# Kernel tuning notes

Hardware: AMD Instinct MI355X
Metric: run time of the kernel (lower is better)

The kernel has to match this reference:

```python
import jax, jax.numpy as jnp
import numpy as np

B, S, H, NH, HD = 2, 2048, 2048, 16, 128


def _bit_linear(x, w):
    """Ternary STE BitLinear: absmean scaling, round/clamp, fp matmul, rescale."""
    eps = 1e-5
    wn = w / (jnp.abs(w).mean() + eps)
    # straight-through estimator: forward uses quantized weights, grad flows to wn
    wq = wn + jax.lax.stop_gradient(jnp.clip(jnp.round(wn), -1.0, 1.0) - wn)
    y = x @ wq.T
    scale = w.shape[1]  # in_features
    Qb = 128.0  # 2**(8-1)
    return jnp.clip(y / scale * Qb, -Qb, Qb)


def _rotate_half(x):
    x1, x2 = jnp.split(x, 2, axis=-1)
    return jnp.concatenate([-x2, x1], axis=-1)


def setup_inputs() -> dict:
    key = jax.random.key(0)
    k1, k2, k3 = jax.random.split(key, 3)
    x = jax.random.normal(k1, (B, S, H), dtype=jnp.float32)
    w_qkv = jax.random.normal(k2, (3 * H, H), dtype=jnp.float32) * 0.02
    w_o = jax.random.normal(k3, (H, H), dtype=jnp.float32) * 0.02
    # realistic RoPE table [2, S, HD]
    inv_freq = 1.0 / (10000.0 ** (jnp.arange(0, HD, 2, dtype=jnp.float32) / HD))
    freqs = jnp.arange(S, dtype=jnp.float32)[:, None] * inv_freq[None, :]
    emb = jnp.concatenate([freqs, freqs], axis=-1)  # [S, HD]
    rotary = jnp.stack([jnp.cos(emb), jnp.sin(emb)], axis=0)
    return {"x": x, "rotary": rotary, "w_qkv": w_qkv, "w_o": w_o}


def reference(x, rotary, w_qkv, w_o):
    qkv = _bit_linear(x, w_qkv)  # [B, S, 3H]
    q, k, v = jnp.split(qkv, 3, axis=-1)
    q = q.reshape(B, S, NH, HD)
    k = k.reshape(B, S, NH, HD)
    v = v.reshape(B, S, NH, HD)
    cos = rotary[0][None, :, None, :]  # [1, S, 1, HD]
    sin = rotary[1][None, :, None, :]
    q = q * cos + _rotate_half(q) * sin
    k = k * cos + _rotate_half(k) * sin
    # [B, NH, S, HD]
    q, k, v = (t.transpose(0, 2, 1, 3) for t in (q, k, v))
    scores = jnp.einsum("bhqd,bhkd->bhqk", q, k) / np.sqrt(HD).astype(np.float32)
    causal = jnp.tril(jnp.ones((S, S), dtype=bool))
    scores = jnp.where(causal[None, None], scores, -jnp.inf)
    attn = jax.nn.softmax(scores, axis=-1)
    y = jnp.einsum("bhqk,bhkd->bhqd", attn, v)
    y = y.transpose(0, 2, 1, 3).reshape(B, S, H)
    return _bit_linear(y, w_o)
```

## Files before the change

### kernel.cpp

```cpp
#include <hip/hip_runtime.h>
#include <hip/hip_bf16.h>
#include <stdint.h>

#define B_   2
#define S_   2048
#define H_   2048
#define NH_  16
#define HD_  128
#define MTOK 4096
#define NQKV 6144

typedef unsigned short u16;
typedef __attribute__((ext_vector_type(8))) __bf16 bf16x8;
typedef __attribute__((ext_vector_type(4))) float f32x4;
typedef __attribute__((ext_vector_type(16))) float f32x16;

static __device__ __forceinline__ float bf2f(u16 u){
  union { uint32_t i; float f; } v; v.i = ((uint32_t)u) << 16; return v.f;
}
static __device__ __forceinline__ u16 f2bf(float f){
  union { float f; uint32_t i; } v; v.f = f;
  uint32_t r = v.i + 0x7FFFu + ((v.i >> 16) & 1u);
  return (u16)(r >> 16);
}
static __device__ __forceinline__ uint32_t cvt_pk_bf16(float lo, float hi){
  uint32_t r;
  asm("v_cvt_pk_bf16_f32 %0, %1, %2" : "=v"(r) : "v"(lo), "v"(hi));
  return r;
}
static __device__ __forceinline__ void pl32swap(uint32_t &a, uint32_t &b){
  asm volatile("v_permlane32_swap_b32 %0, %1" : "+v"(a), "+v"(b));
}

__device__ __forceinline__ void gload_lds16(const void* g, void* l){
  __builtin_amdgcn_global_load_lds((const __attribute__((address_space(1))) void*)g,
                                   (__attribute__((address_space(3))) void*)l, 16, 0, 0);
}

__global__ void absum_kernel(const float* __restrict__ w, int n, float* __restrict__ partial){
  __shared__ float sm[256];
  float s = 0.f;
  for (int i = blockIdx.x*256 + threadIdx.x; i < n; i += gridDim.x*256)
    s += fabsf(w[i]);
  sm[threadIdx.x] = s; __syncthreads();
  for (int st = 128; st > 0; st >>= 1){
    if ((int)threadIdx.x < st) sm[threadIdx.x] += sm[threadIdx.x + st];
    __syncthreads();
  }
  if (threadIdx.x == 0) partial[blockIdx.x] = sm[0];
}

__global__ void finalize_kernel(const float* __restrict__ p1, const float* __restrict__ p2,
                                float* __restrict__ scales){
  __shared__ double sm[256];
  int t = threadIdx.x;
  double s = (double)p1[t] + (double)p1[t+256] + (double)p1[t+512] + (double)p1[t+768];
  sm[t] = s; __syncthreads();
  for (int st = 128; st > 0; st >>= 1){ if (t < st) sm[t] += sm[t+st]; __syncthreads(); }
  if (t == 0) scales[0] = (float)(1.0 / (sm[0] / (double)(3*H_*H_) + 1e-5));
  __syncthreads();
  s = (double)p2[t] + (double)p2[t+256] + (double)p2[t+512] + (double)p2[t+768];
  sm[t] = s; __syncthreads();
  for (int st = 128; st > 0; st >>= 1){ if (t < st) sm[t] += sm[t+st]; __syncthreads(); }
  if (t == 0) scales[1] = (float)(1.0 / (sm[0] / (double)(H_*H_) + 1e-5));
}

__global__ void quant_kernel(const float* __restrict__ w, u16* __restrict__ wq, int n,
                             const float* __restrict__ scales, int which){
  float inv = scales[which];
  for (int i = blockIdx.x*256 + threadIdx.x; i < n; i += gridDim.x*256){
    float q = rintf(w[i] * inv);
    q = fminf(1.f, fmaxf(-1.f, q));
    wq[i] = f2bf(q);
  }
}

__global__ void castx_kernel(const float* __restrict__ x, u16* __restrict__ xb, int n){
  int i = blockIdx.x*256 + threadIdx.x;
  if (i < n) xb[i] = f2bf(x[i]);
}

template<int EPI>
__global__ __launch_bounds__(512, 2) void gemm_kernel(const u16* __restrict__ A,
    const u16* __restrict__ Bw, int M, int N, int K,
    float* __restrict__ outf, u16* __restrict__ qb, u16* __restrict__ kb, u16* __restrict__ vtb)
{
  extern __shared__ u16 lds[];
  int nbm = M >> 7;
  int nb_tot = nbm * (N >> 8);
  int bid = blockIdx.x;
  int chunk = nb_tot >> 3;
  int sb = (bid & 7)*chunk + (bid >> 3);
  int bm = sb % nbm, bn = sb / nbm;
  int m0 = bm << 7, n0 = bn << 8;
  int tid = threadIdx.x;
  int lane = tid & 63, wid = tid >> 6;
  int wm = wid >> 2, wn = wid & 3;
  int lr = lane & 15, lg = lane >> 4;
  int lg8 = lg << 3;
  int kw = (wid & 1) << 5;

  const u16* Ab = A + (size_t)m0 * K;
  const u16* Bb = Bw + (size_t)n0 * K;

  f32x4 acc[4][4];
  #pragma unroll
  for (int i = 0; i < 4; i++)
    #pragma unroll
    for (int j = 0; j < 4; j++) acc[i][j] = f32x4{0.f,0.f,0.f,0.f};

  auto STAGE = [&](int tt, int vlo){
    u16* ldst = lds + (tt % 3) * 24576;
    int k0 = tt << 6;
    #pragma unroll
    for (int v = vlo; v < vlo + 3; v++){
      int f = v*8 + wid;
      const u16* src;
      if (v < 2){
        src = Ab + (size_t)(((f >> 1) << 4) + lr)*K + k0 + kw + lg8;
      } else {
        src = Bb + (size_t)((((f - 16) >> 1) << 4) + lr)*K + k0 + kw + lg8;
      }
      gload_lds16(src, ldst + f*512 + lane*8);
    }
  };

  int NT = K >> 6;
  STAGE(0,0); STAGE(0,3); STAGE(1,0); STAGE(1,3);
  asm volatile("s_waitcnt vmcnt(6)" ::: "memory");
  __builtin_amdgcn_sched_barrier(0);
  __builtin_amdgcn_s_barrier();

  for (int t = 0; t < NT; t++){
    u16* bufp = lds + (t % 3) * 24576;
    #pragma unroll
    for (int ph = 0; ph < 2; ph++){
      if (t + 2 < NT) STAGE(t + 2, ph*3);
      bf16x8 af[4], bfr[4];
      #pragma unroll
      for (int mi = 0; mi < 4; mi++)
        af[mi] = *(const bf16x8*)(bufp + (((wm*4 + mi)*2 + ph)*512) + lane*8);
      #pragma unroll
      for (int ni = 0; ni < 4; ni++)
        bfr[ni] = *(const bf16x8*)(bufp + ((16 + (wn*4 + ni)*2 + ph)*512) + lane*8);
      __builtin_amdgcn_s_setprio(1);
      #pragma unroll
      for (int mi = 0; mi < 4; mi++)
        #pragma unroll
        for (int ni = 0; ni < 4; ni++)
          acc[mi][ni] = __builtin_amdgcn_mfma_f32_16x16x32_bf16(af[mi], bfr[ni], acc[mi][ni], 0, 0, 0);
      __builtin_amdgcn_s_setprio(0);
      if (ph == 0){
        __builtin_amdgcn_s_barrier();
      } else {
        if (t + 2 < NT) asm volatile("s_waitcnt vmcnt(6)" ::: "memory");
        else            asm volatile("s_waitcnt vmcnt(0)" ::: "memory");
        __builtin_amdgcn_sched_barrier(0);
        __builtin_amdgcn_s_barrier();
      }
    }
  }

  #pragma unroll
  for (int mi = 0; mi < 4; mi++){
    #pragma unroll
    for (int ni = 0; ni < 4; ni++){
      int ncol = n0 + wn*64 + ni*16 + lr;
      #pragma unroll
      for (int r = 0; r < 4; r++){
        int m = m0 + wm*64 + mi*16 + lg*4 + r;
        float v = acc[mi][ni][r] * 0.0625f;
        v = fminf(128.f, fmaxf(-128.f, v));
        if (EPI == 1){
          outf[(size_t)m*N + ncol] = v;
        } else {
          int b = m >> 11, s = m & 2047;
          int part = ncol >> 11, c = ncol & 2047;
          int h = c >> 7, d = c & 127;
          int bh = b*NH_ + h;
          u16 bv = f2bf(v);
          if (part == 0)      qb[((bh*S_ + s) << 7) + d] = bv;
          else if (part == 1) kb[((bh*S_ + s) << 7) + d] = bv;
          else                vtb[((bh*HD_ + d) << 11) + s] = bv;
        }
      }
    }
  }
}

__global__ void rope_kernel(u16* __restrict__ qb, u16* __restrict__ kb, const float* __restrict__ rot){
  int i = blockIdx.x*256 + threadIdx.x;
  int d = i & 63;
  int s = (i >> 6) & 2047;
  int bh = (i >> 17) & 31;
  u16* buf = (i >> 22) ? kb : qb;
  int base = (bh*S_ + s)*HD_;
  float c  = rot[s*HD_ + d];
  float sn = rot[S_*HD_ + s*HD_ + d];
  float x1 = bf2f(buf[base + d]);
  float x2 = bf2f(buf[base + d + 64]);
  buf[base + d]      = f2bf(x1*c - x2*sn);
  buf[base + d + 64] = f2bf(x2*c + x1*sn);
}

__global__ __launch_bounds__(256) void attn_kernel(const u16* __restrict__ qb,
    const u16* __restrict__ kb, const u16* __restrict__ vtb, u16* __restrict__ ao)
{
  __shared__ alignas(16) u16 Ks[2][4096];
  __shared__ alignas(16) u16 Vs[2][4096];

  int bid = blockIdx.x;
  int sbid = (bid & 7)*64 + (bid >> 3);
  int bh = sbid >> 4;
  int bq = 15 - (sbid & 15);
  int tid = threadIdx.x;
  int wid = tid >> 6, lane = tid & 63;
  int l31 = lane & 31, hl = lane >> 5;
  int q0 = bq * 128;
  int qw = q0 + wid*32;
  int q  = qw + l31;

  const u16* Qp = qb + (size_t)(bh*S_ + qw)*HD_;
  const u16* Kp = kb + (size_t)bh*S_*HD_;
  const u16* Vt = vtb + (size_t)bh*HD_*S_;

  bf16x8 qf[8];
  #pragma unroll
  for (int t = 0; t < 8; t++)
    qf[t] = *(const bf16x8*)(Qp + l31*HD_ + t*16 + hl*8);

  f32x16 o[4];
  #pragma unroll
  for (int i = 0; i < 4; i++)
    #pragma unroll
    for (int j = 0; j < 16; j++) o[i][j] = 0.f;
  float m_r = -1e30f, l_r = 0.f;
  const float sm_scale = 0.08838834764831845f;

  auto STAGE = [&](int buf, int kt2){
    int t0 = wid*2;
    gload_lds16(Kp + (size_t)(kt2 + l31)*HD_ + (t0  )*16 + hl*8, &Ks[buf][((t0  )*64 + lane)*8]);
    gload_lds16(Kp + (size_t)(kt2 + l31)*HD_ + (t0+1)*16 + hl*8, &Ks[buf][((t0+1)*64 + lane)*8]);
    int v0 = wid*2, v1 = wid*2 + 1;
    gload_lds16(Vt + (size_t)((v0&3)*32 + l31)*S_ + kt2 + (v0>>2)*16 + hl*8, &Vs[buf][(v0*64 + lane)*8]);
    gload_lds16(Vt + (size_t)((v1&3)*32 + l31)*S_ + kt2 + (v1>>2)*16 + hl*8, &Vs[buf][(v1*64 + lane)*8]);
  };

  int n_it = 4*bq + 4;
  STAGE(0, 0);
  int cur = 0, kt = 0;
  for (int it = 0; it < n_it; ++it, kt += 32){
    if (it + 1 < n_it){
      STAGE(cur ^ 1, kt + 32);
      asm volatile("s_waitcnt vmcnt(4)" ::: "memory");
    } else {
      asm volatile("s_waitcnt vmcnt(0)" ::: "memory");
    }
    __builtin_amdgcn_sched_barrier(0);
    __builtin_amdgcn_s_barrier();

    if (kt <= qw){
      f32x16 sa;
      #pragma unroll
      for (int j = 0; j < 16; j++) sa[j] = 0.f;
      #pragma unroll
      for (int t = 0; t < 8; t++){
        bf16x8 kf = *(const bf16x8*)(&Ks[cur][(t*64 + lane)*8]);
        sa = __builtin_amdgcn_mfma_f32_32x32x16_bf16(kf, qf[t], sa, 0, 0, 0);
      }

      float sv[16];
      if (kt == qw){
        #pragma unroll
        for (int r = 0; r < 16; r++){
          int key = kt + (r&3) + 8*(r>>2) + 4*hl;
          sv[r] = (key > q) ? -1e30f : sa[r]*sm_scale;
        }
      } else {
        #pragma unroll
        for (int r = 0; r < 16; r++) sv[r] = sa[r]*sm_scale;
      }

      float pm = sv[0];
      #pragma unroll
      for (int r = 1; r < 16; r++) pm = fmaxf(pm, sv[r]);
      pm = fmaxf(pm, __shfl_xor(pm, 32));
      if (!__all(pm - m_r <= 8.f)){
        float mn = fmaxf(m_r, pm);
        float scl = __expf(m_r - mn);
        m_r = mn; l_r *= scl;
        #pragma unroll
        for (int i = 0; i < 4; i++)
          #pragma unroll
          for (int j = 0; j < 16; j++) o[i][j] *= scl;
      }
      float p[16];
      #pragma unroll
      for (int r = 0; r < 16; r++) p[r] = __expf(sv[r] - m_r);
      float ts = 0.f;
      #pragma unroll
      for (int r = 0; r < 16; r++) ts += p[r];
      ts += __shfl_xor(ts, 32);
      l_r += ts;

      uint32_t a0 = cvt_pk_bf16(p[0],  p[1]),  a1 = cvt_pk_bf16(p[2],  p[3]);
      uint32_t a2 = cvt_pk_bf16(p[4],  p[5]),  a3 = cvt_pk_bf16(p[6],  p[7]);
      uint32_t b0 = cvt_pk_bf16(p[8],  p[9]),  b1 = cvt_pk_bf16(p[10], p[11]);
      uint32_t b2 = cvt_pk_bf16(p[12], p[13]), b3 = cvt_pk_bf16(p[14], p[15]);
      pl32swap(a0, a2); pl32swap(a1, a3);
      pl32swap(b0, b2); pl32swap(b1, b3);
      union { uint32_t u[4]; bf16x8 v; } pf0, pf1;
      pf0.u[0]=a0; pf0.u[1]=a1; pf0.u[2]=a2; pf0.u[3]=a3;
      pf1.u[0]=b0; pf1.u[1]=b1; pf1.u[2]=b2; pf1.u[3]=b3;

      #pragma unroll
      for (int db = 0; db < 4; db++){
        bf16x8 vf0 = *(const bf16x8*)(&Vs[cur][((0*4 + db)*64 + lane)*8]);
        o[db] = __builtin_amdgcn_mfma_f32_32x32x16_bf16(vf0, pf0.v, o[db], 0, 0, 0);
        bf16x8 vf1 = *(const bf16x8*)(&Vs[cur][((1*4 + db)*64 + lane)*8]);
        o[db] = __builtin_amdgcn_mfma_f32_32x32x16_bf16(vf1, pf1.v, o[db], 0, 0, 0);
      }
      asm volatile("s_waitcnt lgkmcnt(0)" ::: "memory");
    }
    __builtin_amdgcn_sched_barrier(0);
    __builtin_amdgcn_s_barrier();
    cur ^= 1;
  }

  float inv = 1.f / l_r;
  int b = bh >> 4, hh = bh & 15;
  u16* orow = ao + (size_t)(b*S_ + q)*H_ + hh*HD_;
  #pragma unroll
  for (int db = 0; db < 4; db++){
    #pragma unroll
    for (int g = 0; g < 4; g++){
      ushort4 pk4;
      pk4.x = f2bf(o[db][4*g+0]*inv);
      pk4.y = f2bf(o[db][4*g+1]*inv);
      pk4.z = f2bf(o[db][4*g+2]*inv);
      pk4.w = f2bf(o[db][4*g+3]*inv);
      *(ushort4*)(orow + db*32 + g*8 + hl*4) = pk4;
    }
  }
}

extern "C" void kernel_launch(void* const* d_in, const int* in_sizes, int n_in,
                              void* d_out, int out_size, void* d_ws, size_t ws_size,
                              hipStream_t stream) {
  const float* x      = (const float*)d_in[0];
  const float* rotary = (const float*)d_in[1];
  const float* w_qkv  = (const float*)d_in[2];
  const float* w_o    = (const float*)d_in[3];
  float* out = (float*)d_out;

  char* wsb = (char*)d_ws;
  float* part_qkv = (float*)wsb;
  float* part_o   = part_qkv + 1024;
  float* scales   = part_o + 1024;
  size_t off = 16384;
  u16* xb    = (u16*)(wsb + off); off += (size_t)MTOK*H_*2;
  u16* wqkvq = (u16*)(wsb + off); off += (size_t)NQKV*H_*2;
  u16* woq   = (u16*)(wsb + off); off += (size_t)H_*H_*2;
  u16* qbuf  = (u16*)(wsb + off); off += (size_t)B_*NH_*S_*HD_*2;
  u16* kbuf  = (u16*)(wsb + off); off += (size_t)B_*NH_*S_*HD_*2;
  u16* vtb   = (u16*)(wsb + off); off += (size_t)B_*NH_*S_*HD_*2;
  u16* ao    = (u16*)(wsb + off); off += (size_t)MTOK*H_*2;

  const int GEMM_LDS = 3 * 48 * 1024;
  hipFuncSetAttribute((const void*)&gemm_kernel<0>,
                      hipFuncAttributeMaxDynamicSharedMemorySize, GEMM_LDS);
  hipFuncSetAttribute((const void*)&gemm_kernel<1>,
                      hipFuncAttributeMaxDynamicSharedMemorySize, GEMM_LDS);

  absum_kernel<<<1024, 256, 0, stream>>>(w_qkv, 3*H_*H_, part_qkv);
  absum_kernel<<<1024, 256, 0, stream>>>(w_o, H_*H_, part_o);
  finalize_kernel<<<1, 256, 0, stream>>>(part_qkv, part_o, scales);
  quant_kernel<<<4096, 256, 0, stream>>>(w_qkv, wqkvq, 3*H_*H_, scales, 0);
  quant_kernel<<<2048, 256, 0, stream>>>(w_o, woq, H_*H_, scales, 1);
  castx_kernel<<<(MTOK*H_)/256, 256, 0, stream>>>(x, xb, MTOK*H_);

  gemm_kernel<0><<<(MTOK/128)*(NQKV/256), 512, GEMM_LDS, stream>>>(xb, wqkvq, MTOK, NQKV, H_,
                                                                   nullptr, qbuf, kbuf, vtb);
  rope_kernel<<<(2*B_*NH_*S_*64)/256, 256, 0, stream>>>(qbuf, kbuf, rotary);
  attn_kernel<<<B_*NH_*(S_/128), 256, 0, stream>>>(qbuf, kbuf, vtb, ao);
  gemm_kernel<1><<<(MTOK/128)*(H_/256), 512, GEMM_LDS, stream>>>(ao, woq, MTOK, H_, H_,
                                                                 out, nullptr, nullptr, nullptr);
}
```

Baseline: 421.4 us.

## Enlarge GEMM tiles to 256x256 with double-buffered 8-wave ping-pong schedule

The bf16 GEMM goes from 128x256 to 256x256 block tiles, so each wave holds an 8x4 grid of 16x16 accumulators. The triple-buffered K=64 pipeline becomes a double-buffered even/odd LDS scheme. Global-to-LDS staging is interleaved with quarter-tile MFMA groups between barriers, with fine-grained vmcnt and lgkmcnt waits. This aims to raise arithmetic intensity and cut global traffic per FLOP, in exchange for more registers, 128KB of LDS (so likely one block per CU), fewer blocks and many extra barriers.

Result: slower. 439.5 us (+4.3%).

```diff
diff --git a/kernel.cpp b/kernel.cpp
--- a/kernel.cpp
+++ b/kernel.cpp
@@ -80,95 +80,135 @@
   if (i < n) xb[i] = f2bf(x[i]);
 }
 
+#define BARR  __builtin_amdgcn_s_barrier()
+#define LGKM0 asm volatile("s_waitcnt lgkmcnt(0)" ::: "memory")
+#define VMW4  do{ asm volatile("s_waitcnt vmcnt(4)" ::: "memory"); __builtin_amdgcn_sched_barrier(0); }while(0)
+#define VMW0  do{ asm volatile("s_waitcnt vmcnt(0)" ::: "memory"); __builtin_amdgcn_sched_barrier(0); }while(0)
+
+#define LDA4(basep, MI0) do{                                           \
+  _Pragma("unroll") for (int mi = 0; mi < 4; mi++)                     \
+    _Pragma("unroll") for (int ks = 0; ks < 2; ks++)                   \
+      aR[mi][ks] = *(const bf16x8*)((basep) +                          \
+          (((wm*8 + (MI0) + mi)*2 + ks)<<9) + (lane<<3));              \
+}while(0)
+#define LDB2(basep, DST, NI0) do{                                      \
+  _Pragma("unroll") for (int ni = 0; ni < 2; ni++)                     \
+    _Pragma("unroll") for (int ks = 0; ks < 2; ks++)                   \
+      DST[ni][ks] = *(const bf16x8*)((basep) +                         \
+          (((wn*4 + (NI0) + ni)*2 + ks)<<9) + (lane<<3));              \
+}while(0)
+#define MMQ(Aa, Bb2, MI0, NI0) do{                                     \
+  __builtin_amdgcn_s_setprio(1);                                       \
+  _Pragma("unroll") for (int ks = 0; ks < 2; ks++)                     \
+    _Pragma("unroll") for (int mi = 0; mi < 4; mi++)                   \
+      _Pragma("unroll") for (int ni = 0; ni < 2; ni++)                 \
+        acc[(MI0)+mi][(NI0)+ni] = __builtin_amdgcn_mfma_f32_16x16x32_bf16( \
+            Aa[mi][ks], Bb2[ni][ks], acc[(MI0)+mi][(NI0)+ni], 0, 0, 0);\
+  __builtin_amdgcn_s_setprio(0);                                       \
+}while(0)
+
 template<int EPI>
 __global__ __launch_bounds__(512, 2) void gemm_kernel(const u16* __restrict__ A,
     const u16* __restrict__ Bw, int M, int N, int K,
     float* __restrict__ outf, u16* __restrict__ qb, u16* __restrict__ kb, u16* __restrict__ vtb)
 {
   extern __shared__ u16 lds[];
-  int nbm = M >> 7;
+  const int AE = 0, BE = 16384, AO = 32768, BO = 49152;
+  int nbm = M >> 8;
   int nb_tot = nbm * (N >> 8);
   int bid = blockIdx.x;
   int chunk = nb_tot >> 3;
   int sb = (bid & 7)*chunk + (bid >> 3);
   int bm = sb % nbm, bn = sb / nbm;
-  int m0 = bm << 7, n0 = bn << 8;
+  int m0 = bm << 8, n0 = bn << 8;
   int tid = threadIdx.x;
   int lane = tid & 63, wid = tid >> 6;
   int wm = wid >> 2, wn = wid & 3;
   int lr = lane & 15, lg = lane >> 4;
   int lg8 = lg << 3;
-  int kw = (wid & 1) << 5;
 
   const u16* Ab = A + (size_t)m0 * K;
   const u16* Bb = Bw + (size_t)n0 * K;
 
-  f32x4 acc[4][4];
+  f32x4 acc[8][4];
   #pragma unroll
-  for (int i = 0; i < 4; i++)
+  for (int i = 0; i < 8; i++)
     #pragma unroll
     for (int j = 0; j < 4; j++) acc[i][j] = f32x4{0.f,0.f,0.f,0.f};
 
-  auto STAGE = [&](int tt, int vlo){
-    u16* ldst = lds + (tt % 3) * 24576;
-    int k0 = tt << 6;
-    #pragma unroll
-    for (int v = vlo; v < vlo + 3; v++){
-      int f = v*8 + wid;
-      const u16* src;
-      if (v < 2){
-        src = Ab + (size_t)(((f >> 1) << 4) + lr)*K + k0 + kw + lg8;
-      } else {
-        src = Bb + (size_t)((((f - 16) >> 1) << 4) + lr)*K + k0 + kw + lg8;
-      }
-      gload_lds16(src, ldst + f*512 + lane*8);
+  auto STAGE_A = [&](int T, int h){
+    u16* base = lds + ((T & 1) ? AO : AE);
+    int kt = T << 6;
+    #pragma unroll
+    for (int j = 0; j < 2; j++){
+      int fa = h*16 + wid*2 + j;
+      int m16 = fa >> 1, ks = fa & 1;
+      gload_lds16(Ab + (size_t)(m16*16 + lr)*K + kt + ks*32 + lg8,
+                  base + (fa<<9) + (lane<<3));
     }
   };
-
-  int NT = K >> 6;
-  STAGE(0,0); STAGE(0,3); STAGE(1,0); STAGE(1,3);
-  asm volatile("s_waitcnt vmcnt(6)" ::: "memory");
-  __builtin_amdgcn_sched_barrier(0);
-  __builtin_amdgcn_s_barrier();
-
-  for (int t = 0; t < NT; t++){
-    u16* bufp = lds + (t % 3) * 24576;
-    #pragma unroll
-    for (int ph = 0; ph < 2; ph++){
-      if (t + 2 < NT) STAGE(t + 2, ph*3);
-      bf16x8 af[4], bfr[4];
-      #pragma unroll
-      for (int mi = 0; mi < 4; mi++)
-        af[mi] = *(const bf16x8*)(bufp + (((wm*4 + mi)*2 + ph)*512) + lane*8);
-      #pragma unroll
-      for (int ni = 0; ni < 4; ni++)
-        bfr[ni] = *(const bf16x8*)(bufp + ((16 + (wn*4 + ni)*2 + ph)*512) + lane*8);
-      __builtin_amdgcn_s_setprio(1);
-      #pragma unroll
-      for (int mi = 0; mi < 4; mi++)
-        #pragma unroll
-        for (int ni = 0; ni < 4; ni++)
-          acc[mi][ni] = __builtin_amdgcn_mfma_f32_16x16x32_bf16(af[mi], bfr[ni], acc[mi][ni], 0, 0, 0);
-      __builtin_amdgcn_s_setprio(0);
-      if (ph == 0){
-        __builtin_amdgcn_s_barrier();
-      } else {
-        if (t + 2 < NT) asm volatile("s_waitcnt vmcnt(6)" ::: "memory");
-        else            asm volatile("s_waitcnt vmcnt(0)" ::: "memory");
-        __builtin_amdgcn_sched_barrier(0);
-        __builtin_amdgcn_s_barrier();
-      }
-    }
+  auto STAGE_B = [&](int T, int h){
+    u16* base = lds + ((T & 1) ? BO : BE);
+    int kt = T << 6;
+    #pragma unroll
+    for (int j = 0; j < 2; j++){
+      int fb = h*16 + wid*2 + j;
+      int n16 = fb >> 1, ks = fb & 1;
+      gload_lds16(Bb + (size_t)(n16*16 + lr)*K + kt + ks*32 + lg8,
+                  base + (fb<<9) + (lane<<3));
+    }
+  };
+
+  const u16* aE = lds + AE; const u16* bE = lds + BE;
+  const u16* aO = lds + AO; const u16* bO = lds + BO;
+
+  STAGE_A(0,0); STAGE_A(0,1); STAGE_B(0,0); STAGE_B(0,1);
+  STAGE_B(1,0); STAGE_A(1,0);
+  VMW4;
+  BARR;
+
+  int NITER = K >> 7;
+  for (int i = 0; i < NITER; i++){
+    bool last = (i == NITER - 1);
+    int t1 = 2*i + 1, t2 = 2*i + 2, t3 = 2*i + 3;
+    bf16x8 aR[4][2], bLo[2][2], bHi[2][2];
+
+    LDA4(aE, 0); LDB2(bE, bLo, 0);
+    STAGE_B(t1, 1);
+    BARR; LGKM0; MMQ(aR, bLo, 0, 0); BARR;
+    LDB2(bE, bHi, 2);
+    STAGE_A(t1, 1);
+    BARR; LGKM0; MMQ(aR, bHi, 0, 2); BARR;
+    LDA4(aE, 4);
+    if (!last) STAGE_B(t2, 0);
+    BARR; LGKM0; MMQ(aR, bHi, 4, 2); BARR;
+    if (!last) STAGE_A(t2, 0);
+    BARR; LGKM0; MMQ(aR, bLo, 4, 0);
+    if (!last) VMW4; else VMW0;
+    BARR;
+    LDA4(aO, 0); LDB2(bO, bLo, 0);
+    if (!last) STAGE_B(t2, 1);
+    BARR; LGKM0; MMQ(aR, bLo, 0, 0); BARR;
+    LDB2(bO, bHi, 2);
+    if (!last) STAGE_A(t2, 1);
+    BARR; LGKM0; MMQ(aR, bHi, 0, 2); BARR;
+    LDA4(aO, 4);
+    if (!last) STAGE_B(t3, 0);
+    BARR; LGKM0; MMQ(aR, bHi, 4, 2); BARR;
+    if (!last) STAGE_A(t3, 0);
+    BARR; LGKM0; MMQ(aR, bLo, 4, 0);
+    if (!last){ VMW4; }
+    BARR;
   }
 
   #pragma unroll
-  for (int mi = 0; mi < 4; mi++){
+  for (int mi = 0; mi < 8; mi++){
     #pragma unroll
     for (int ni = 0; ni < 4; ni++){
       int ncol = n0 + wn*64 + ni*16 + lr;
       #pragma unroll
       for (int r = 0; r < 4; r++){
-        int m = m0 + wm*64 + mi*16 + lg*4 + r;
+        int m = m0 + wm*128 + mi*16 + lg*4 + r;
         float v = acc[mi][ni][r] * 0.0625f;
         v = fminf(128.f, fmaxf(-128.f, v));
         if (EPI == 1){
@@ -366,7 +406,7 @@
   u16* vtb   = (u16*)(wsb + off); off += (size_t)B_*NH_*S_*HD_*2;
   u16* ao    = (u16*)(wsb + off); off += (size_t)MTOK*H_*2;
 
-  const int GEMM_LDS = 3 * 48 * 1024;
+  const int GEMM_LDS = 128 * 1024;
   hipFuncSetAttribute((const void*)&gemm_kernel<0>,
                       hipFuncAttributeMaxDynamicSharedMemorySize, GEMM_LDS);
   hipFuncSetAttribute((const void*)&gemm_kernel<1>,
@@ -379,10 +419,10 @@
   quant_kernel<<<2048, 256, 0, stream>>>(w_o, woq, H_*H_, scales, 1);
   castx_kernel<<<(MTOK*H_)/256, 256, 0, stream>>>(x, xb, MTOK*H_);
 
-  gemm_kernel<0><<<(MTOK/128)*(NQKV/256), 512, GEMM_LDS, stream>>>(xb, wqkvq, MTOK, NQKV, H_,
+  gemm_kernel<0><<<(MTOK/256)*(NQKV/256), 512, GEMM_LDS, stream>>>(xb, wqkvq, MTOK, NQKV, H_,
                                                                    nullptr, qbuf, kbuf, vtb);
   rope_kernel<<<(2*B_*NH_*S_*64)/256, 256, 0, stream>>>(qbuf, kbuf, rotary);
   attn_kernel<<<B_*NH_*(S_/128), 256, 0, stream>>>(qbuf, kbuf, vtb, ao);
-  gemm_kernel<1><<<(MTOK/128)*(H_/256), 512, GEMM_LDS, stream>>>(ao, woq, MTOK, H_, H_,
+  gemm_kernel<1><<<(MTOK/256)*(H_/256), 512, GEMM_LDS, stream>>>(ao, woq, MTOK, H_, H_,
                                                                  out, nullptr, nullptr, nullptr);
 }
```
